# Kernel tuning notes

Measured on AMD Instinct MI355X. Metric: run time of the kernel, lower is better.

Reference implementation:

```python
import jax, jax.numpy as jnp
import numpy as np

B, C, H, W = 4, 512, 32, 32
NH = 8
HD = C // NH
PH, PW = 2, 4
NPR = PH * PW
HIDDEN = int(C * 2.0)
EPS = 1e-5

def _bn(x, p):
    g, b, m, v = p[0], p[1], p[2], p[3]
    s = g * jax.lax.rsqrt(v + EPS)
    return x * s[None, :, None, None] + (b - m * s)[None, :, None, None]

def _ln(x, p):
    mu = x.mean(-1, keepdims=True)
    var = ((x - mu) ** 2).mean(-1, keepdims=True)
    return (x - mu) * jax.lax.rsqrt(var + EPS) * p[0] + p[1]

def _dwconv(x, w):
    return jax.lax.conv_general_dilated(
        x, w, (1, 1), 'SAME',
        dimension_numbers=('NCHW', 'OIHW', 'NCHW'),
        feature_group_count=x.shape[1])

def _pw(x, w):
    # 1x1 conv, no bias: w is (O, I, 1, 1)
    return jnp.einsum('bchw,oc->bohw', x, w[:, :, 0, 0])

def _pool(x, ph, pw):
    # adaptive avg pool when output evenly divides input
    b, c, h, w = x.shape
    return x.reshape(b, c, ph, h // ph, pw, w // pw).mean(axis=(3, 5))

def _gelu(x):
    return jax.nn.gelu(x, approximate=False)

def _coords(h, w):
    y = jnp.linspace(0.0, 1.0, h)
    x = jnp.linspace(0.0, 1.0, w)
    gy, gx = jnp.meshgrid(y, x, indexing='ij')
    return jnp.stack([gy, gx], axis=-1).reshape(-1, 2)


def setup_inputs() -> dict:
    key = jax.random.key(0)
    ks = iter(jax.random.split(key, 64))
    def nrm(shape, s=0.02):
        return jax.random.normal(next(ks), shape, jnp.float32) * s
    def bnp():
        return jnp.stack([1.0 + nrm((C,), 0.1), nrm((C,), 0.1),
                          nrm((C,), 0.1), 1.0 + jnp.abs(nrm((C,), 0.2))])
    def lnp(c=C):
        return jnp.stack([jnp.ones((c,), jnp.float32), jnp.zeros((c,), jnp.float32)])
    return {
        'fused': jax.random.normal(next(ks), (B, C, H, W), jnp.float32),
        'depth': jax.random.normal(next(ks), (B, C, H, W), jnp.float32),
        'pg_dw_w': nrm((C, 1, 3, 3)), 'pg_bn1': bnp(),
        'pg_pw_w': nrm((C, C, 1, 1)), 'pg_bn2': bnp(),
        'prompt_embed': nrm((1, NPR, C)), 'pg_ln': lnp(),
        'gp_dw_w': nrm((C, 1, 3, 3)), 'gp_bn': bnp(),
        'gp_pw_w': nrm((1, C, 1, 1)), 'gp_pw_b': jnp.zeros((1,), jnp.float32),
        'gp_weight': jnp.ones((2, 1, 1, 1), jnp.float32),
        'ln1': lnp(),
        'wq': nrm((C, C)), 'wk': nrm((C, C)), 'wv': nrm((C, C)), 'wo': nrm((C, C)),
        'ln2': lnp(),
        'mlp_w1': nrm((HIDDEN, C)), 'mlp_b1': jnp.zeros((HIDDEN,), jnp.float32),
        'mlp_w2': nrm((C, HIDDEN)), 'mlp_b2': jnp.zeros((C,), jnp.float32),
        'op_dw_w': nrm((C, 1, 3, 3)), 'op_bn1': bnp(),
        'op_pw_w': nrm((C, C, 1, 1)), 'op_bn2': bnp(),
    }


def reference(fused, depth, pg_dw_w, pg_bn1, pg_pw_w, pg_bn2, prompt_embed, pg_ln,
              gp_dw_w, gp_bn, gp_pw_w, gp_pw_b, gp_weight,
              ln1, wq, wk, wv, wo, ln2, mlp_w1, mlp_b1, mlp_w2, mlp_b2,
              op_dw_w, op_bn1, op_pw_w, op_bn2):
    b = fused.shape[0]
    # --- DepthPromptGenerator ---
    pp = _gelu(_bn(_dwconv(depth, pg_dw_w), pg_bn1))
    pp = _gelu(_bn(_pw(pp, pg_pw_w), pg_bn2))
    prompt = _pool(pp, PH, PW).reshape(b, C, NPR).transpose(0, 2, 1)  # (B, P, C)
    prompt = _ln(prompt + prompt_embed, pg_ln)
    # --- GeometryPriorGenerator ---
    ds = _gelu(_bn(_dwconv(depth, gp_dw_w), gp_bn))
    ds = _pw(ds, gp_pw_w) + gp_pw_b[None, :, None, None]  # (B,1,H,W)
    img_d = ds.reshape(b, H * W)
    pr_d = _pool(ds, PH, PW).reshape(b, NPR)
    jd = jnp.concatenate([pr_d, img_d], axis=1)  # (B, N) depth scalar per token
    coords = jnp.concatenate([_coords(PH, PW), _coords(H, W)], axis=0)  # (N,2)
    pos = jnp.abs(coords[:, None, :] - coords[None, :, :]).sum(-1)  # (N,N) L1 distance
    decay = jnp.log(1.0 - 2.0 ** (-1.0 - 4.0 * jnp.arange(NH, dtype=jnp.float32) / NH))
    pos_mask = pos[None, :, :] * decay[:, None, None]  # (NH,N,N)
    depth_mask = jnp.abs(jd[:, :, None] - jd[:, None, :])[:, None, :, :] * decay[None, :, None, None]
    bias = gp_weight[0, 0, 0, 0] * pos_mask[None] + gp_weight[1, 0, 0, 0] * depth_mask  # (B,NH,N,N)
    # --- GeometryAwarePromptMixer ---
    img_tok = fused.reshape(b, C, H * W).transpose(0, 2, 1)  # (B,HW,C)
    jt = jnp.concatenate([prompt, img_tok], axis=1)  # (B,N,C)
    n = jt.shape[1]
    x = _ln(jt, ln1)
    q = jnp.einsum('bnc,dc->bnd', x, wq).reshape(b, n, NH, HD).transpose(0, 2, 1, 3)
    k = jnp.einsum('bnc,dc->bnd', x, wk).reshape(b, n, NH, HD).transpose(0, 2, 1, 3)
    v = jnp.einsum('bnc,dc->bnd', x, wv).reshape(b, n, NH, HD).transpose(0, 2, 1, 3)
    logits = jnp.einsum('bhnd,bhmd->bhnm', q, k) * (HD ** -0.5) + bias
    attn = jax.nn.softmax(logits, axis=-1)
    ao = jnp.einsum('bhnm,bhmd->bhnd', attn, v).transpose(0, 2, 1, 3).reshape(b, n, C)
    jt = jt + jnp.einsum('bnc,dc->bnd', ao, wo)
    h = _gelu(jnp.einsum('bnc,hc->bnh', _ln(jt, ln2), mlp_w1) + mlp_b1)
    jt = jt + jnp.einsum('bnh,ch->bnc', h, mlp_w2) + mlp_b2
    enh = jt[:, NPR:, :].transpose(0, 2, 1).reshape(b, C, H, W)
    # --- out_proj ---
    o = _gelu(_bn(_dwconv(enh, op_dw_w), op_bn1))
    o = _bn(_pw(o, op_pw_w), op_bn2)
    return fused + o
```

## Files before the change

kernel.cpp:

```cpp
#include <hip/hip_runtime.h>
#include <math.h>

typedef __attribute__((ext_vector_type(8))) short bf16x8;
typedef __attribute__((ext_vector_type(4))) float f32x4;

#define CH 512
#define HWP 1024
#define NTOK 1032
#define NTP 1088
#define NPRM 8
#define BB 4
#define EPSV 1e-5f
#define MTOK 4128
#define MPAD 4224
#define QSCL 0.18033688f
#define LOG2E 1.44269504f

__device__ __forceinline__ float gelu_f(float x) {
  return 0.5f * x * (1.0f + erff(x * 0.70710678118654752440f));
}

__device__ __forceinline__ ushort f2bf(float x) {
  union { float f; unsigned u; } v; v.f = x;
  unsigned r = v.u + 0x7FFF + ((v.u >> 16) & 1);
  return (ushort)(r >> 16);
}

__device__ __forceinline__ float bf2f(ushort u) {
  union { unsigned u; float f; } v; v.u = ((unsigned)u) << 16;
  return v.f;
}

__device__ __forceinline__ void gl16(const ushort* g, ushort* s) {
  __builtin_amdgcn_global_load_lds(
      (const __attribute__((address_space(1))) unsigned int*)g,
      (__attribute__((address_space(3))) unsigned int*)s,
      16, 0, 0);
}

__global__ __launch_bounds__(256) void convw(
    const float* __restrict__ wq, const float* __restrict__ wk, const float* __restrict__ wv,
    const float* __restrict__ wo, const float* __restrict__ w1, const float* __restrict__ w2,
    const float* __restrict__ pgw, const float* __restrict__ opw, const float* __restrict__ gpw,
    ushort* __restrict__ out)
{
  const int total = 2621952;
  for (int i = blockIdx.x * 256 + threadIdx.x; i < total; i += gridDim.x * 256) {
    const float* src; int off;
    if (i < 262144)       { src = wq;  off = i; }
    else if (i < 524288)  { src = wk;  off = i - 262144; }
    else if (i < 786432)  { src = wv;  off = i - 524288; }
    else if (i < 1048576) { src = wo;  off = i - 786432; }
    else if (i < 1572864) { src = w1;  off = i - 1048576; }
    else if (i < 2097152) { src = w2;  off = i - 1572864; }
    else if (i < 2359296) { src = pgw; off = i - 2097152; }
    else if (i < 2621440) { src = opw; off = i - 2359296; }
    else                  { src = gpw; off = i - 2621440; }
    out[i] = f2bf(src[off]);
  }
}

__global__ __launch_bounds__(256) void dwt_fused(
    const float* __restrict__ in, const float* __restrict__ w9p,
    const float* __restrict__ bn, ushort* __restrict__ outT)
{
  __shared__ float tile[32][33];
  const int y = blockIdx.x;
  const int c0 = blockIdx.y * 32;
  const int b = blockIdx.z;
  const int tx = threadIdx.x, ty = threadIdx.y;
  #pragma unroll
  for (int i = 0; i < 4; ++i) {
    int c = c0 + ty + i * 8;
    const float* ip = in + ((size_t)(b * CH + c)) * HWP;
    const float* wp = w9p + c * 9;
    float acc = 0.0f;
    #pragma unroll
    for (int dy = 0; dy < 3; ++dy) {
      int yy = y + dy - 1;
      if ((unsigned)yy < 32u) {
        #pragma unroll
        for (int dx = 0; dx < 3; ++dx) {
          int xx = tx + dx - 1;
          if ((unsigned)xx < 32u) acc += ip[yy * 32 + xx] * wp[dy * 3 + dx];
        }
      }
    }
    float g = bn[c], be = bn[CH + c], mm = bn[2 * CH + c], vv = bn[3 * CH + c];
    float s = g * rsqrtf(vv + EPSV);
    tile[ty + i * 8][tx] = gelu_f(acc * s + (be - mm * s));
  }
  __syncthreads();
  #pragma unroll
  for (int i = 0; i < 4; ++i)
    outT[((size_t)(b * HWP + y * 32 + ty + i * 8)) * CH + c0 + tx] = f2bf(tile[tx][ty + i * 8]);
}

__device__ __forceinline__ void stage128(const ushort* pA, const ushort* pB,
                                         ushort* lA, ushort* lB,
                                         int w, int KA, int KB)
{
  #pragma unroll
  for (int j = 0; j < 4; ++j) {
    gl16(pA + (size_t)j * 8 * KA, lA + (w * 32 + j * 8) * 64);
    gl16(pB + (size_t)j * 8 * KB, lB + (w * 32 + j * 8) * 64);
  }
}

__device__ __forceinline__ void comp128(const ushort* lA, const ushort* lB,
                                        int wm, int wn, int l, f32x4 (&acc)[4][4])
{
  #pragma unroll
  for (int ks = 0; ks < 2; ++ks) {
    int kb = ks * 4 + (l >> 4);
    int swz = ((kb ^ (l & 7)) * 8);
    bf16x8 af[4], bfv[4];
    #pragma unroll
    for (int mf = 0; mf < 4; ++mf)
      af[mf] = *(const bf16x8*)(lA + (wm + mf * 16 + (l & 15)) * 64 + swz);
    #pragma unroll
    for (int nf = 0; nf < 4; ++nf)
      bfv[nf] = *(const bf16x8*)(lB + (wn + nf * 16 + (l & 15)) * 64 + swz);
    #pragma unroll
    for (int mf = 0; mf < 4; ++mf) {
      #pragma unroll
      for (int nf = 0; nf < 4; ++nf)
        acc[mf][nf] = __builtin_amdgcn_mfma_f32_16x16x32_bf16(af[mf], bfv[nf], acc[mf][nf], 0, 0, 0);
    }
  }
}

#define G128_PRE(Abase, Bbase, KA, KB, Kdim) \
  __shared__ ushort sA[2][8192], sB[2][8192]; \
  f32x4 acc[4][4]; \
  { f32x4 z = {0.f, 0.f, 0.f, 0.f}; \
    _Pragma("unroll") for (int i = 0; i < 4; ++i) { _Pragma("unroll") for (int j = 0; j < 4; ++j) acc[i][j] = z; } } \
  const int l = threadIdx.x & 63, w = threadIdx.x >> 6; \
  const int wm = (w >> 1) * 64, wn = (w & 1) * 64; \
  const ushort* pA = (Abase) + (size_t)(w * 32 + (l >> 3)) * (KA) + ((l & 7) ^ (l >> 3)) * 8; \
  const ushort* pB = (Bbase) + (size_t)(w * 32 + (l >> 3)) * (KB) + ((l & 7) ^ (l >> 3)) * 8; \
  stage128(pA, pB, sA[0], sB[0], w, KA, KB); \
  __syncthreads(); \
  const int nk = (Kdim) / 64; \
  for (int kt = 0; kt < nk; ++kt) { \
    if (kt + 1 < nk) \
      stage128(pA + (kt + 1) * 64, pB + (kt + 1) * 64, sA[(kt + 1) & 1], sB[(kt + 1) & 1], w, KA, KB); \
    comp128(sA[kt & 1], sB[kt & 1], wm, wn, l, acc); \
    __syncthreads(); \
  }

__global__ __launch_bounds__(256) void gemm_qkv128(
    const ushort* __restrict__ A, const ushort* __restrict__ B,
    ushort* __restrict__ qh, ushort* __restrict__ kh, ushort* __restrict__ vt)
{
  const int n0 = blockIdx.x * 128, m0 = blockIdx.y * 128;
  G128_PRE(A + (size_t)m0 * 512, B + (size_t)n0 * 512, 512, 512, 512)
  #pragma unroll
  for (int nf = 0; nf < 4; ++nf) {
    int n = n0 + wn + nf * 16 + (l & 15);
    #pragma unroll
    for (int mf = 0; mf < 4; ++mf) {
      #pragma unroll
      for (int r = 0; r < 4; ++r) {
        int m = m0 + wm + mf * 16 + (l >> 4) * 4 + r;
        if (m < MTOK) {
          int b = m / NTOK;
          int tok = m - b * NTOK;
          float val = acc[mf][nf][r];
          if (n < 512) {
            qh[((size_t)((b * 8 + (n >> 6)) * NTP) + tok) * 64 + (n & 63)] = f2bf(val * QSCL);
          } else if (n < 1024) {
            int n2 = n - 512;
            kh[((size_t)((b * 8 + (n2 >> 6)) * NTP) + tok) * 64 + (n2 & 63)] = f2bf(val);
          } else {
            int n2 = n - 1024;
            vt[((size_t)((b * 8 + (n2 >> 6)) * 64) + (n2 & 63)) * NTP + tok] = f2bf(val);
          }
        }
      }
    }
  }
}

__global__ __launch_bounds__(256) void gemm_res128(
    const ushort* __restrict__ A, const ushort* __restrict__ B,
    float* __restrict__ Cf, const float* __restrict__ bias, int Kdim)
{
  const int n0 = blockIdx.x * 128, m0 = blockIdx.y * 128;
  G128_PRE(A + (size_t)m0 * Kdim, B + (size_t)n0 * Kdim, Kdim, Kdim, Kdim)
  #pragma unroll
  for (int nf = 0; nf < 4; ++nf) {
    int n = n0 + wn + nf * 16 + (l & 15);
    float bv = bias ? bias[n] : 0.0f;
    #pragma unroll
    for (int mf = 0; mf < 4; ++mf) {
      #pragma unroll
      for (int r = 0; r < 4; ++r) {
        int m = m0 + wm + mf * 16 + (l >> 4) * 4 + r;
        if (m < MTOK) Cf[(size_t)m * 512 + n] += acc[mf][nf][r] + bv;
      }
    }
  }
}

__global__ __launch_bounds__(256) void gemm_gelu128(
    const ushort* __restrict__ A, const ushort* __restrict__ B,
    const float* __restrict__ bias, ushort* __restrict__ Ob)
{
  const int n0 = blockIdx.x * 128, m0 = blockIdx.y * 128;
  G128_PRE(A + (size_t)m0 * 512, B + (size_t)n0 * 512, 512, 512, 512)
  #pragma unroll
  for (int nf = 0; nf < 4; ++nf) {
    int n = n0 + wn + nf * 16 + (l & 15);
    float bv = bias[n];
    #pragma unroll
    for (int mf = 0; mf < 4; ++mf) {
      #pragma unroll
      for (int r = 0; r < 4; ++r) {
        int m = m0 + wm + mf * 16 + (l >> 4) * 4 + r;
        if (m < MTOK) Ob[(size_t)m * 1024 + n] = f2bf(gelu_f(acc[mf][nf][r] + bv));
      }
    }
  }
}

template<int MODE>
__global__ __launch_bounds__(256) void gemm_pw128(
    const ushort* __restrict__ A, const ushort* __restrict__ B,
    const float* __restrict__ bnp, const float* __restrict__ res, float* __restrict__ Of)
{
  const int hw0 = blockIdx.x * 128, m0 = blockIdx.y * 128;
  const int b = blockIdx.z;
  G128_PRE(A + (size_t)m0 * 512, B + (size_t)(b * HWP + hw0) * 512, 512, 512, 512)
  #pragma unroll
  for (int mf = 0; mf < 4; ++mf) {
    #pragma unroll
    for (int r = 0; r < 4; ++r) {
      int o = m0 + wm + mf * 16 + (l >> 4) * 4 + r;
      float g = bnp[o], be = bnp[CH + o], mm = bnp[2 * CH + o], vv = bnp[3 * CH + o];
      float s = g * rsqrtf(vv + EPSV);
      float sh = be - mm * s;
      #pragma unroll
      for (int nf = 0; nf < 4; ++nf) {
        int hw = hw0 + wn + nf * 16 + (l & 15);
        float x = acc[mf][nf][r] * s + sh;
        size_t oi = ((size_t)(b * CH + o)) * HWP + hw;
        if (MODE == 0) Of[oi] = gelu_f(x);
        else Of[oi] = x + res[oi];
      }
    }
  }
}

__global__ __launch_bounds__(128) void pp_pool(const float* __restrict__ pp, float* __restrict__ ppool)
{
  int bc = blockIdx.x;
  int b = bc >> 9, c = bc & 511;
  __shared__ float sums[8];
  if (threadIdx.x < 8) sums[threadIdx.x] = 0.0f;
  __syncthreads();
  const float* ip = pp + (size_t)bc * HWP;
  float s0 = 0.0f, s1 = 0.0f;
  #pragma unroll
  for (int kq = 0; kq < 8; ++kq) {
    float val = ip[threadIdx.x + kq * 128];
    if (kq < 4) s0 += val; else s1 += val;
  }
  int pxr = (threadIdx.x & 31) >> 3;
  atomicAdd(&sums[pxr], s0);
  atomicAdd(&sums[4 + pxr], s1);
  __syncthreads();
  if (threadIdx.x < 8)
    ppool[((size_t)b * 8 + threadIdx.x) * CH + c] = sums[threadIdx.x] * (1.0f / 128.0f);
}

__global__ __launch_bounds__(128) void prompt_ln(
    const float* __restrict__ ppool, const float* __restrict__ embed,
    const float* __restrict__ lnp, float* __restrict__ jt)
{
  int rB = blockIdx.x;
  int b = rB >> 3, pI = rB & 7;
  float4 val = ((const float4*)(ppool + (size_t)rB * CH))[threadIdx.x];
  float4 e = ((const float4*)(embed + (size_t)pI * CH))[threadIdx.x];
  val.x += e.x; val.y += e.y; val.z += e.z; val.w += e.w;
  float sum = val.x + val.y + val.z + val.w;
  float sq = val.x * val.x + val.y * val.y + val.z * val.z + val.w * val.w;
  #pragma unroll
  for (int off = 1; off < 64; off <<= 1) { sum += __shfl_xor(sum, off); sq += __shfl_xor(sq, off); }
  __shared__ float s2[4];
  if ((threadIdx.x & 63) == 0) { s2[(threadIdx.x >> 6) * 2] = sum; s2[(threadIdx.x >> 6) * 2 + 1] = sq; }
  __syncthreads();
  sum = s2[0] + s2[2]; sq = s2[1] + s2[3];
  float mu = sum * (1.0f / 512.0f);
  float var = sq * (1.0f / 512.0f) - mu * mu;
  float rstd = rsqrtf(var + EPSV);
  int c = threadIdx.x * 4;
  float4 o;
  o.x = (val.x - mu) * rstd * lnp[c] + lnp[CH + c];
  o.y = (val.y - mu) * rstd * lnp[c + 1] + lnp[CH + c + 1];
  o.z = (val.z - mu) * rstd * lnp[c + 2] + lnp[CH + c + 2];
  o.w = (val.w - mu) * rstd * lnp[c + 3] + lnp[CH + c + 3];
  ((float4*)(jt + ((size_t)(b * NTOK + pI)) * CH))[threadIdx.x] = o;
}

__global__ __launch_bounds__(256) void gp_dot(
    const ushort* __restrict__ xT, const ushort* __restrict__ wbf,
    const float* __restrict__ b0, float* __restrict__ jdv)
{
  const int b = blockIdx.y;
  const int row0 = blockIdx.x * 16;
  const int l = threadIdx.x & 63, w = threadIdx.x >> 6;
  bf16x8 wv = *(const bf16x8*)(wbf + l * 8);
  float wf[8];
  #pragma unroll
  for (int j = 0; j < 8; ++j) wf[j] = bf2f((ushort)wv[j]);
  #pragma unroll
  for (int rr = 0; rr < 4; ++rr) {
    int hw = row0 + w * 4 + rr;
    bf16x8 xv = *(const bf16x8*)(xT + ((size_t)(b * HWP + hw)) * CH + l * 8);
    float s = 0.0f;
    #pragma unroll
    for (int j = 0; j < 8; ++j) s += wf[j] * bf2f((ushort)xv[j]);
    #pragma unroll
    for (int off = 1; off < 64; off <<= 1) s += __shfl_xor(s, off);
    if (l == 0) jdv[b * NTP + NPRM + hw] = s + b0[0];
  }
}

__global__ __launch_bounds__(256) void jd_pool(float* jd)
{
  int b = blockIdx.x;
  __shared__ float sums[8];
  if (threadIdx.x < 8) sums[threadIdx.x] = 0.0f;
  __syncthreads();
  #pragma unroll
  for (int kq = 0; kq < 4; ++kq) {
    int px = threadIdx.x + kq * 256;
    int y = px >> 5, x = px & 31;
    int r = (y >> 4) * 4 + (x >> 3);
    atomicAdd(&sums[r], jd[b * NTP + NPRM + px]);
  }
  __syncthreads();
  if (threadIdx.x < 8) jd[b * NTP + threadIdx.x] = sums[threadIdx.x] * (1.0f / 128.0f);
}

__global__ __launch_bounds__(256) void img_to_tokens(const float* __restrict__ fused, float* __restrict__ jt)
{
  __shared__ float tile[32][33];
  int hw0 = blockIdx.x * 32, c0 = blockIdx.y * 32, b = blockIdx.z;
  int tx = threadIdx.x, ty = threadIdx.y;
  #pragma unroll
  for (int i = 0; i < 4; ++i)
    tile[ty + i * 8][tx] = fused[((size_t)(b * CH + c0 + ty + i * 8)) * HWP + hw0 + tx];
  __syncthreads();
  #pragma unroll
  for (int i = 0; i < 4; ++i)
    jt[((size_t)(b * NTOK + NPRM + hw0 + ty + i * 8)) * CH + c0 + tx] = tile[tx][ty + i * 8];
}

__global__ __launch_bounds__(256) void tokens_to_img(const float* __restrict__ jt, float* __restrict__ out)
{
  __shared__ float tile[32][33];
  int hw0 = blockIdx.x * 32, c0 = blockIdx.y * 32, b = blockIdx.z;
  int tx = threadIdx.x, ty = threadIdx.y;
  #pragma unroll
  for (int i = 0; i < 4; ++i)
    tile[ty + i * 8][tx] = jt[((size_t)(b * NTOK + NPRM + hw0 + ty + i * 8)) * CH + c0 + tx];
  __syncthreads();
  #pragma unroll
  for (int i = 0; i < 4; ++i)
    out[((size_t)(b * CH + c0 + ty + i * 8)) * HWP + hw0 + tx] = tile[tx][ty + i * 8];
}

__global__ __launch_bounds__(128) void ln_rows_bf(
    const float* __restrict__ in, const float* __restrict__ lnp, ushort* __restrict__ out)
{
  int row = blockIdx.x;
  float4 val = ((const float4*)(in + (size_t)row * CH))[threadIdx.x];
  float sum = val.x + val.y + val.z + val.w;
  float sq = val.x * val.x + val.y * val.y + val.z * val.z + val.w * val.w;
  #pragma unroll
  for (int off = 1; off < 64; off <<= 1) { sum += __shfl_xor(sum, off); sq += __shfl_xor(sq, off); }
  __shared__ float s2[4];
  if ((threadIdx.x & 63) == 0) { s2[(threadIdx.x >> 6) * 2] = sum; s2[(threadIdx.x >> 6) * 2 + 1] = sq; }
  __syncthreads();
  sum = s2[0] + s2[2]; sq = s2[1] + s2[3];
  float mu = sum * (1.0f / 512.0f);
  float var = sq * (1.0f / 512.0f) - mu * mu;
  float rstd = rsqrtf(var + EPSV);
  int c = threadIdx.x * 4;
  ushort4 o;
  o.x = f2bf((val.x - mu) * rstd * lnp[c] + lnp[CH + c]);
  o.y = f2bf((val.y - mu) * rstd * lnp[c + 1] + lnp[CH + c + 1]);
  o.z = f2bf((val.z - mu) * rstd * lnp[c + 2] + lnp[CH + c + 2]);
  o.w = f2bf((val.w - mu) * rstd * lnp[c + 3] + lnp[CH + c + 3]);
  *(ushort4*)(out + (size_t)row * CH + c) = o;
}

__device__ __forceinline__ void tok_coord(int idx, float& y, float& x)
{
  if (idx < NPRM) { y = (float)(idx >> 2); x = (float)(idx & 3) * (1.0f / 3.0f); }
  else { int t = idx - NPRM; y = (float)(t >> 5) * (1.0f / 31.0f); x = (float)(t & 31) * (1.0f / 31.0f); }
}

__global__ __launch_bounds__(256) void attn_mfma2(
    const ushort* __restrict__ qh, const ushort* __restrict__ kh,
    const ushort* __restrict__ vT, const float* __restrict__ jd,
    const float* __restrict__ gw, ushort* __restrict__ ao)
{
  __shared__ ushort sK[8192], sV[8192];
  __shared__ ushort Pl[4][16][72];
  const int t = threadIdx.x, l = t & 63, w = t >> 6;
  const int h = blockIdx.y, b = blockIdx.z;
  const int i0 = blockIdx.x * 64 + w * 16;
  const ushort* Q = qh + (size_t)(b * 8 + h) * NTP * 64;
  const ushort* K = kh + (size_t)(b * 8 + h) * NTP * 64;
  const ushort* V = vT + (size_t)(b * 8 + h) * 64 * NTP;
  const float decay = logf(1.0f - exp2f(-1.0f - 0.5f * (float)h)) * LOG2E;
  const float g0 = gw[0] * decay, g1 = gw[1] * decay;

  bf16x8 qf0 = *(const bf16x8*)(Q + (size_t)(i0 + (l & 15)) * 64 + (l >> 4) * 8);
  bf16x8 qf1 = *(const bf16x8*)(Q + (size_t)(i0 + (l & 15)) * 64 + 32 + (l >> 4) * 8);

  float yi[4], xi[4], jdi[4];
  #pragma unroll
  for (int r = 0; r < 4; ++r) {
    int i = i0 + (l >> 4) * 4 + r;
    tok_coord(i, yi[r], xi[r]);
    jdi[r] = jd[b * NTP + i];
  }

  float m_r[4] = { -1e30f, -1e30f, -1e30f, -1e30f };
  float l_r[4] = { 0.f, 0.f, 0.f, 0.f };
  f32x4 of[4];
  { f32x4 z = {0.f, 0.f, 0.f, 0.f};
    #pragma unroll
    for (int d = 0; d < 4; ++d) of[d] = z; }

#define ASTAGE(buf, j0s) { \
    const ushort* gk = K + (size_t)((j0s) + l) * 64; \
    const ushort* gv = V + (size_t)l * NTP + (j0s); \
    gl16(gk + w * 8,       sK + (buf) * 4096 + w * 512); \
    gl16(gk + (w + 4) * 8, sK + (buf) * 4096 + (w + 4) * 512); \
    gl16(gv + w * 8,       sV + (buf) * 4096 + w * 512); \
    gl16(gv + (w + 4) * 8, sV + (buf) * 4096 + (w + 4) * 512); }

  ASTAGE(0, 0)
  __syncthreads();
  const int NJT = 17;
  for (int jti = 0; jti < NJT; ++jti) {
    const int j0 = jti * 64;
    if (jti + 1 < NJT) ASTAGE((jti + 1) & 1, j0 + 64)
    const ushort* bK = sK + (jti & 1) * 4096;
    const ushort* bV = sV + (jti & 1) * 4096;

    f32x4 sfr[4];
    #pragma unroll
    for (int jf = 0; jf < 4; ++jf) {
      bf16x8 k0 = *(const bf16x8*)(bK + (((l >> 4)) * 64 + jf * 16 + (l & 15)) * 8);
      bf16x8 k1 = *(const bf16x8*)(bK + ((4 + (l >> 4)) * 64 + jf * 16 + (l & 15)) * 8);
      f32x4 z = {0.f, 0.f, 0.f, 0.f};
      z = __builtin_amdgcn_mfma_f32_16x16x32_bf16(qf0, k0, z, 0, 0, 0);
      z = __builtin_amdgcn_mfma_f32_16x16x32_bf16(qf1, k1, z, 0, 0, 0);
      sfr[jf] = z;
    }
    float pvv[4][4];
    float mt[4] = { -1e30f, -1e30f, -1e30f, -1e30f };
    #pragma unroll
    for (int jf = 0; jf < 4; ++jf) {
      int jj = j0 + jf * 16 + (l & 15);
      float yj, xj;
      tok_coord(jj, yj, xj);
      float jdj = jd[b * NTP + jj];
      bool valid = jj < NTOK;
      #pragma unroll
      for (int r = 0; r < 4; ++r) {
        float bias = g0 * (fabsf(yi[r] - yj) + fabsf(xi[r] - xj)) + g1 * fabsf(jdi[r] - jdj);
        float sv = valid ? (sfr[jf][r] + bias) : -1e30f;
        pvv[jf][r] = sv;
        mt[r] = fmaxf(mt[r], sv);
      }
    }
    #pragma unroll
    for (int r = 0; r < 4; ++r) {
      #pragma unroll
      for (int off = 1; off < 16; off <<= 1) mt[r] = fmaxf(mt[r], __shfl_xor(mt[r], off));
    }
    float alpha[4], ls[4];
    #pragma unroll
    for (int r = 0; r < 4; ++r) {
      float mn = fmaxf(m_r[r], mt[r]);
      alpha[r] = exp2f(m_r[r] - mn);
      m_r[r] = mn;
      ls[r] = 0.f;
    }
    #pragma unroll
    for (int jf = 0; jf < 4; ++jf) {
      #pragma unroll
      for (int r = 0; r < 4; ++r) {
        float pp = exp2f(pvv[jf][r] - m_r[r]);
        pvv[jf][r] = pp;
        ls[r] += pp;
      }
    }
    #pragma unroll
    for (int r = 0; r < 4; ++r) {
      #pragma unroll
      for (int off = 1; off < 16; off <<= 1) ls[r] += __shfl_xor(ls[r], off);
      l_r[r] = l_r[r] * alpha[r] + ls[r];
    }
    #pragma unroll
    for (int d = 0; d < 4; ++d) {
      #pragma unroll
      for (int r = 0; r < 4; ++r) of[d][r] *= alpha[r];
    }
    #pragma unroll
    for (int jf = 0; jf < 4; ++jf) {
      #pragma unroll
      for (int r = 0; r < 4; ++r)
        Pl[w][(l >> 4) * 4 + r][jf * 16 + (l & 15)] = f2bf(pvv[jf][r]);
    }
    asm volatile("s_waitcnt lgkmcnt(0)" ::: "memory");
    bf16x8 pa0 = *(const bf16x8*)&Pl[w][l & 15][(l >> 4) * 8];
    bf16x8 pa1 = *(const bf16x8*)&Pl[w][l & 15][32 + (l >> 4) * 8];
    #pragma unroll
    for (int df = 0; df < 4; ++df) {
      bf16x8 v0 = *(const bf16x8*)(bV + (((l >> 4)) * 64 + df * 16 + (l & 15)) * 8);
      bf16x8 v1 = *(const bf16x8*)(bV + ((4 + (l >> 4)) * 64 + df * 16 + (l & 15)) * 8);
      of[df] = __builtin_amdgcn_mfma_f32_16x16x32_bf16(pa0, v0, of[df], 0, 0, 0);
      of[df] = __builtin_amdgcn_mfma_f32_16x16x32_bf16(pa1, v1, of[df], 0, 0, 0);
    }
    __syncthreads();
  }
  #pragma unroll
  for (int r = 0; r < 4; ++r) {
    int i = i0 + (l >> 4) * 4 + r;
    if (i < NTOK) {
      float inv = 1.0f / l_r[r];
      #pragma unroll
      for (int df = 0; df < 4; ++df)
        ao[((size_t)(b * NTOK + i)) * 512 + h * 64 + df * 16 + (l & 15)] = f2bf(of[df][r] * inv);
    }
  }
}

extern "C" void kernel_launch(void* const* d_in, const int* in_sizes, int n_in,
                              void* d_out, int out_size, void* d_ws, size_t ws_size,
                              hipStream_t stream)
{
  const float* fused = (const float*)d_in[0];
  const float* depth = (const float*)d_in[1];
  const float* pg_dw_w = (const float*)d_in[2];
  const float* pg_bn1 = (const float*)d_in[3];
  const float* pg_pw_w = (const float*)d_in[4];
  const float* pg_bn2 = (const float*)d_in[5];
  const float* prompt_embed = (const float*)d_in[6];
  const float* pg_ln = (const float*)d_in[7];
  const float* gp_dw_w = (const float*)d_in[8];
  const float* gp_bn = (const float*)d_in[9];
  const float* gp_pw_w = (const float*)d_in[10];
  const float* gp_pw_b = (const float*)d_in[11];
  const float* gp_weight = (const float*)d_in[12];
  const float* ln1 = (const float*)d_in[13];
  const float* wq = (const float*)d_in[14];
  const float* wk = (const float*)d_in[15];
  const float* wv = (const float*)d_in[16];
  const float* wo = (const float*)d_in[17];
  const float* ln2 = (const float*)d_in[18];
  const float* mlp_w1 = (const float*)d_in[19];
  const float* mlp_b1 = (const float*)d_in[20];
  const float* mlp_w2 = (const float*)d_in[21];
  const float* mlp_b2 = (const float*)d_in[22];
  const float* op_dw_w = (const float*)d_in[23];
  const float* op_bn1 = (const float*)d_in[24];
  const float* op_pw_w = (const float*)d_in[25];
  const float* op_bn2 = (const float*)d_in[26];
  float* out = (float*)d_out;

  char* p = (char*)d_ws;
  auto alloc = [&](size_t bytes) { char* r = p; p += (bytes + 1023) & ~(size_t)1023; return r; };
  float*  jt    = (float*) alloc((size_t)MTOK * 512 * 4);
  ushort* xb    = (ushort*)alloc((size_t)MPAD * 512 * 2);
  ushort* hb    = (ushort*)alloc((size_t)MPAD * 1024 * 2);
  ushort* ao    = (ushort*)alloc((size_t)MPAD * 512 * 2);
  ushort* qhB   = (ushort*)alloc((size_t)32 * NTP * 64 * 2);
  ushort* khB   = (ushort*)alloc((size_t)32 * NTP * 64 * 2);
  ushort* vTB   = (ushort*)alloc((size_t)32 * NTP * 64 * 2);
  ushort* dwT1  = (ushort*)alloc((size_t)BB * HWP * CH * 2);
  ushort* dwT2  = (ushort*)alloc((size_t)BB * HWP * CH * 2);
  float*  ppf   = (float*) alloc((size_t)BB * CH * HWP * 4);
  float*  Bf    = (float*) alloc((size_t)BB * CH * HWP * 4);
  float*  jdv   = (float*) alloc((size_t)BB * NTP * 4);
  float*  ppool = (float*) alloc((size_t)BB * 8 * CH * 4);
  ushort* wbf   = (ushort*)alloc((size_t)2621952 * 2);

  ushort* wqkv_bf = wbf;
  ushort* wo_bf   = wbf + 786432;
  ushort* w1_bf   = wbf + 1048576;
  ushort* w2_bf   = wbf + 1572864;
  ushort* pgw_bf  = wbf + 2097152;
  ushort* opw_bf  = wbf + 2359296;
  ushort* gpw_bf  = wbf + 2621440;

  hipLaunchKernelGGL(convw, dim3(4096), dim3(256), 0, stream,
                     wq, wk, wv, wo, mlp_w1, mlp_w2, pg_pw_w, op_pw_w, gp_pw_w, wbf);

  hipLaunchKernelGGL(dwt_fused, dim3(32, 16, BB), dim3(32, 8), 0, stream, depth, pg_dw_w, pg_bn1, dwT1);
  hipLaunchKernelGGL(gemm_pw128<0>, dim3(8, 4, BB), dim3(256), 0, stream, pgw_bf, dwT1, pg_bn2, (const float*)nullptr, ppf);
  hipLaunchKernelGGL(pp_pool, dim3(BB * CH), dim3(128), 0, stream, ppf, ppool);
  hipLaunchKernelGGL(prompt_ln, dim3(BB * NPRM), dim3(128), 0, stream, ppool, prompt_embed, pg_ln, jt);

  hipLaunchKernelGGL(dwt_fused, dim3(32, 16, BB), dim3(32, 8), 0, stream, depth, gp_dw_w, gp_bn, dwT2);
  hipLaunchKernelGGL(gp_dot, dim3(64, BB), dim3(256), 0, stream, dwT2, gpw_bf, gp_pw_b, jdv);
  hipLaunchKernelGGL(jd_pool, dim3(BB), dim3(256), 0, stream, jdv);

  hipLaunchKernelGGL(img_to_tokens, dim3(32, 16, BB), dim3(32, 8), 0, stream, fused, jt);
  hipLaunchKernelGGL(ln_rows_bf, dim3(MTOK), dim3(128), 0, stream, jt, ln1, xb);
  hipLaunchKernelGGL(gemm_qkv128, dim3(12, 33), dim3(256), 0, stream, xb, wqkv_bf, qhB, khB, vTB);
  hipLaunchKernelGGL(attn_mfma2, dim3(17, 8, BB), dim3(256), 0, stream, qhB, khB, vTB, jdv, gp_weight, ao);
  hipLaunchKernelGGL(gemm_res128, dim3(4, 33), dim3(256), 0, stream, ao, wo_bf, jt, (const float*)nullptr, 512);
  hipLaunchKernelGGL(ln_rows_bf, dim3(MTOK), dim3(128), 0, stream, jt, ln2, xb);
  hipLaunchKernelGGL(gemm_gelu128, dim3(8, 33), dim3(256), 0, stream, xb, w1_bf, mlp_b1, hb);
  hipLaunchKernelGGL(gemm_res128, dim3(4, 33), dim3(256), 0, stream, hb, w2_bf, jt, mlp_b2, 1024);

  hipLaunchKernelGGL(tokens_to_img, dim3(32, 16, BB), dim3(32, 8), 0, stream, jt, Bf);
  hipLaunchKernelGGL(dwt_fused, dim3(32, 16, BB), dim3(32, 8), 0, stream, Bf, op_dw_w, op_bn1, dwT1);
  hipLaunchKernelGGL(gemm_pw128<1>, dim3(8, 4, BB), dim3(256), 0, stream, opw_bf, dwT1, op_bn2, fused, out);
}
```

Baseline: 390.3 us.

## Fuse preprocessing stages: dual depthwise conv, pooled pointwise GEMM, combined token/LN kernel

Computes both depthwise convolutions on the depth input in one pass and fuses the prompt pointwise GEMM with GELU and region pooling through shared-memory and global atomics, so the full-resolution fp32 intermediate is never written. It also merges image-to-token transpose, LN1, prompt LN, the geometry dot product and its pooling into one multi-role kernel. The output depthwise conv now reads the token layout directly, dropping the tokens-to-image transpose. The convw grid is halved and zeroing memsets are added. These changes cut kernel launches and large fp32 round trips, at the cost of atomic contention, float-atomic ordering nondeterminism, and a combined kernel whose roles are unevenly loaded.

```diff
diff --git a/kernel.cpp b/kernel.cpp
--- a/kernel.cpp
+++ b/kernel.cpp
@@ -60,11 +60,14 @@
   }
 }
 
-__global__ __launch_bounds__(256) void dwt_fused(
-    const float* __restrict__ in, const float* __restrict__ w9p,
-    const float* __restrict__ bn, ushort* __restrict__ outT)
-{
-  __shared__ float tile[32][33];
+__global__ __launch_bounds__(256) void dwt_dual(
+    const float* __restrict__ in,
+    const float* __restrict__ w1p, const float* __restrict__ bn1,
+    const float* __restrict__ w2p, const float* __restrict__ bn2,
+    ushort* __restrict__ o1, ushort* __restrict__ o2)
+{
+  __shared__ float t1[32][33];
+  __shared__ float t2[32][33];
   const int y = blockIdx.x;
   const int c0 = blockIdx.y * 32;
   const int b = blockIdx.z;
@@ -73,8 +76,9 @@
   for (int i = 0; i < 4; ++i) {
     int c = c0 + ty + i * 8;
     const float* ip = in + ((size_t)(b * CH + c)) * HWP;
-    const float* wp = w9p + c * 9;
-    float acc = 0.0f;
+    const float* wa = w1p + c * 9;
+    const float* wb = w2p + c * 9;
+    float a1 = 0.0f, a2 = 0.0f;
     #pragma unroll
     for (int dy = 0; dy < 3; ++dy) {
       int yy = y + dy - 1;
@@ -82,18 +86,28 @@
         #pragma unroll
         for (int dx = 0; dx < 3; ++dx) {
           int xx = tx + dx - 1;
-          if ((unsigned)xx < 32u) acc += ip[yy * 32 + xx] * wp[dy * 3 + dx];
+          if ((unsigned)xx < 32u) {
+            float v = ip[yy * 32 + xx];
+            a1 += v * wa[dy * 3 + dx];
+            a2 += v * wb[dy * 3 + dx];
+          }
         }
       }
     }
-    float g = bn[c], be = bn[CH + c], mm = bn[2 * CH + c], vv = bn[3 * CH + c];
-    float s = g * rsqrtf(vv + EPSV);
-    tile[ty + i * 8][tx] = gelu_f(acc * s + (be - mm * s));
+    float g1 = bn1[c], be1 = bn1[CH + c], m1 = bn1[2 * CH + c], v1 = bn1[3 * CH + c];
+    float s1 = g1 * rsqrtf(v1 + EPSV);
+    t1[ty + i * 8][tx] = gelu_f(a1 * s1 + (be1 - m1 * s1));
+    float g2 = bn2[c], be2 = bn2[CH + c], m2 = bn2[2 * CH + c], v2 = bn2[3 * CH + c];
+    float s2 = g2 * rsqrtf(v2 + EPSV);
+    t2[ty + i * 8][tx] = gelu_f(a2 * s2 + (be2 - m2 * s2));
   }
   __syncthreads();
   #pragma unroll
-  for (int i = 0; i < 4; ++i)
-    outT[((size_t)(b * HWP + y * 32 + ty + i * 8)) * CH + c0 + tx] = f2bf(tile[tx][ty + i * 8]);
+  for (int i = 0; i < 4; ++i) {
+    size_t row = (size_t)(b * HWP + y * 32 + ty + i * 8) * CH + c0 + tx;
+    o1[row] = f2bf(t1[tx][ty + i * 8]);
+    o2[row] = f2bf(t2[tx][ty + i * 8]);
+  }
 }
 
 __device__ __forceinline__ void stage128(const ushort* pA, const ushort* pB,
@@ -224,8 +238,53 @@
   }
 }
 
-template<int MODE>
-__global__ __launch_bounds__(256) void gemm_pw128(
+__global__ __launch_bounds__(256) void gemm_pw_pool(
+    const ushort* __restrict__ A, const ushort* __restrict__ B,
+    const float* __restrict__ bnp, float* __restrict__ ppool)
+{
+  __shared__ float poolL[8][128];
+  const int hw0 = blockIdx.x * 128, m0 = blockIdx.y * 128;
+  const int b = blockIdx.z;
+  {
+    int t = threadIdx.x;
+    #pragma unroll
+    for (int k = 0; k < 4; ++k) { int idx = t + k * 256; poolL[idx >> 7][idx & 127] = 0.0f; }
+  }
+  G128_PRE(A + (size_t)m0 * 512, B + (size_t)(b * HWP + hw0) * 512, 512, 512, 512)
+  #pragma unroll
+  for (int mf = 0; mf < 4; ++mf) {
+    #pragma unroll
+    for (int r = 0; r < 4; ++r) {
+      int ol = wm + mf * 16 + (l >> 4) * 4 + r;
+      int o = m0 + ol;
+      float g = bnp[o], be = bnp[CH + o], mm = bnp[2 * CH + o], vv = bnp[3 * CH + o];
+      float s = g * rsqrtf(vv + EPSV);
+      float sh = be - mm * s;
+      #pragma unroll
+      for (int nf = 0; nf < 4; ++nf) {
+        int hw = hw0 + wn + nf * 16 + (l & 15);
+        float x = gelu_f(acc[mf][nf][r] * s + sh);
+        int y = hw >> 5, xx = hw & 31;
+        int rg = (y >> 4) * 4 + (xx >> 3);
+        atomicAdd(&poolL[rg][ol], x);
+      }
+    }
+  }
+  __syncthreads();
+  {
+    int t = threadIdx.x;
+    #pragma unroll
+    for (int k = 0; k < 4; ++k) {
+      int idx = t + k * 256;
+      int rg = idx >> 7, oo = idx & 127;
+      float v = poolL[rg][oo];
+      if (v != 0.0f)
+        atomicAdd(&ppool[((size_t)(b * 8 + rg)) * 512 + m0 + oo], v * (1.0f / 128.0f));
+    }
+  }
+}
+
+__global__ __launch_bounds__(256) void gemm_pw_res(
     const ushort* __restrict__ A, const ushort* __restrict__ B,
     const float* __restrict__ bnp, const float* __restrict__ res, float* __restrict__ Of)
 {
@@ -243,133 +302,116 @@
       #pragma unroll
       for (int nf = 0; nf < 4; ++nf) {
         int hw = hw0 + wn + nf * 16 + (l & 15);
-        float x = acc[mf][nf][r] * s + sh;
         size_t oi = ((size_t)(b * CH + o)) * HWP + hw;
-        if (MODE == 0) Of[oi] = gelu_f(x);
-        else Of[oi] = x + res[oi];
-      }
-    }
-  }
-}
-
-__global__ __launch_bounds__(128) void pp_pool(const float* __restrict__ pp, float* __restrict__ ppool)
-{
-  int bc = blockIdx.x;
-  int b = bc >> 9, c = bc & 511;
-  __shared__ float sums[8];
-  if (threadIdx.x < 8) sums[threadIdx.x] = 0.0f;
-  __syncthreads();
-  const float* ip = pp + (size_t)bc * HWP;
-  float s0 = 0.0f, s1 = 0.0f;
-  #pragma unroll
-  for (int kq = 0; kq < 8; ++kq) {
-    float val = ip[threadIdx.x + kq * 128];
-    if (kq < 4) s0 += val; else s1 += val;
-  }
-  int pxr = (threadIdx.x & 31) >> 3;
-  atomicAdd(&sums[pxr], s0);
-  atomicAdd(&sums[4 + pxr], s1);
-  __syncthreads();
-  if (threadIdx.x < 8)
-    ppool[((size_t)b * 8 + threadIdx.x) * CH + c] = sums[threadIdx.x] * (1.0f / 128.0f);
-}
-
-__global__ __launch_bounds__(128) void prompt_ln(
-    const float* __restrict__ ppool, const float* __restrict__ embed,
-    const float* __restrict__ lnp, float* __restrict__ jt)
-{
-  int rB = blockIdx.x;
-  int b = rB >> 3, pI = rB & 7;
-  float4 val = ((const float4*)(ppool + (size_t)rB * CH))[threadIdx.x];
-  float4 e = ((const float4*)(embed + (size_t)pI * CH))[threadIdx.x];
-  val.x += e.x; val.y += e.y; val.z += e.z; val.w += e.w;
-  float sum = val.x + val.y + val.z + val.w;
-  float sq = val.x * val.x + val.y * val.y + val.z * val.z + val.w * val.w;
-  #pragma unroll
-  for (int off = 1; off < 64; off <<= 1) { sum += __shfl_xor(sum, off); sq += __shfl_xor(sq, off); }
-  __shared__ float s2[4];
-  if ((threadIdx.x & 63) == 0) { s2[(threadIdx.x >> 6) * 2] = sum; s2[(threadIdx.x >> 6) * 2 + 1] = sq; }
-  __syncthreads();
-  sum = s2[0] + s2[2]; sq = s2[1] + s2[3];
-  float mu = sum * (1.0f / 512.0f);
-  float var = sq * (1.0f / 512.0f) - mu * mu;
-  float rstd = rsqrtf(var + EPSV);
-  int c = threadIdx.x * 4;
-  float4 o;
-  o.x = (val.x - mu) * rstd * lnp[c] + lnp[CH + c];
-  o.y = (val.y - mu) * rstd * lnp[c + 1] + lnp[CH + c + 1];
-  o.z = (val.z - mu) * rstd * lnp[c + 2] + lnp[CH + c + 2];
-  o.w = (val.w - mu) * rstd * lnp[c + 3] + lnp[CH + c + 3];
-  ((float4*)(jt + ((size_t)(b * NTOK + pI)) * CH))[threadIdx.x] = o;
-}
-
-__global__ __launch_bounds__(256) void gp_dot(
-    const ushort* __restrict__ xT, const ushort* __restrict__ wbf,
+        Of[oi] = acc[mf][nf][r] * s + sh + res[oi];
+      }
+    }
+  }
+}
+
+__global__ __launch_bounds__(256) void combo_mid(
+    const float* __restrict__ fused, const float* __restrict__ ppool,
+    const float* __restrict__ embed, const float* __restrict__ pgln,
+    const float* __restrict__ ln1, float* __restrict__ jt, ushort* __restrict__ xb,
+    const ushort* __restrict__ dwT2, const ushort* __restrict__ gpw,
     const float* __restrict__ b0, float* __restrict__ jdv)
 {
-  const int b = blockIdx.y;
-  const int row0 = blockIdx.x * 16;
-  const int l = threadIdx.x & 63, w = threadIdx.x >> 6;
-  bf16x8 wv = *(const bf16x8*)(wbf + l * 8);
-  float wf[8];
-  #pragma unroll
-  for (int j = 0; j < 8; ++j) wf[j] = bf2f((ushort)wv[j]);
-  #pragma unroll
-  for (int rr = 0; rr < 4; ++rr) {
-    int hw = row0 + w * 4 + rr;
-    bf16x8 xv = *(const bf16x8*)(xT + ((size_t)(b * HWP + hw)) * CH + l * 8);
-    float s = 0.0f;
-    #pragma unroll
-    for (int j = 0; j < 8; ++j) s += wf[j] * bf2f((ushort)xv[j]);
-    #pragma unroll
-    for (int off = 1; off < 64; off <<= 1) s += __shfl_xor(s, off);
-    if (l == 0) jdv[b * NTP + NPRM + hw] = s + b0[0];
-  }
-}
-
-__global__ __launch_bounds__(256) void jd_pool(float* jd)
-{
-  int b = blockIdx.x;
-  __shared__ float sums[8];
-  if (threadIdx.x < 8) sums[threadIdx.x] = 0.0f;
-  __syncthreads();
-  #pragma unroll
-  for (int kq = 0; kq < 4; ++kq) {
-    int px = threadIdx.x + kq * 256;
-    int y = px >> 5, x = px & 31;
-    int r = (y >> 4) * 4 + (x >> 3);
-    atomicAdd(&sums[r], jd[b * NTP + NPRM + px]);
-  }
-  __syncthreads();
-  if (threadIdx.x < 8) jd[b * NTP + threadIdx.x] = sums[threadIdx.x] * (1.0f / 128.0f);
-}
-
-__global__ __launch_bounds__(256) void img_to_tokens(const float* __restrict__ fused, float* __restrict__ jt)
-{
-  __shared__ float tile[32][33];
-  int hw0 = blockIdx.x * 32, c0 = blockIdx.y * 32, b = blockIdx.z;
-  int tx = threadIdx.x, ty = threadIdx.y;
-  #pragma unroll
-  for (int i = 0; i < 4; ++i)
-    tile[ty + i * 8][tx] = fused[((size_t)(b * CH + c0 + ty + i * 8)) * HWP + hw0 + tx];
-  __syncthreads();
-  #pragma unroll
-  for (int i = 0; i < 4; ++i)
-    jt[((size_t)(b * NTOK + NPRM + hw0 + ty + i * 8)) * CH + c0 + tx] = tile[tx][ty + i * 8];
-}
-
-__global__ __launch_bounds__(256) void tokens_to_img(const float* __restrict__ jt, float* __restrict__ out)
-{
-  __shared__ float tile[32][33];
-  int hw0 = blockIdx.x * 32, c0 = blockIdx.y * 32, b = blockIdx.z;
-  int tx = threadIdx.x, ty = threadIdx.y;
-  #pragma unroll
-  for (int i = 0; i < 4; ++i)
-    tile[ty + i * 8][tx] = jt[((size_t)(b * NTOK + NPRM + hw0 + ty + i * 8)) * CH + c0 + tx];
-  __syncthreads();
-  #pragma unroll
-  for (int i = 0; i < 4; ++i)
-    out[((size_t)(b * CH + c0 + ty + i * 8)) * HWP + hw0 + tx] = tile[tx][ty + i * 8];
+  __shared__ float T[32][513];
+  __shared__ float red[16];
+  const int t = threadIdx.x;
+  const int bx = blockIdx.x;
+  if (bx < 128) {
+    int b = bx >> 5, hw0 = (bx & 31) * 32;
+    int tx = t & 31, ty = t >> 5;
+    #pragma unroll
+    for (int cc = 0; cc < 512; cc += 8)
+      T[tx][cc + ty] = fused[((size_t)(b * 512 + cc + ty)) * 1024 + hw0 + tx];
+    __syncthreads();
+    int tok = t >> 3, j = t & 7;
+    float s = 0.f, sq = 0.f;
+    #pragma unroll
+    for (int i = 0; i < 64; ++i) {
+      float v = T[tok][j * 64 + i];
+      s += v; sq += v * v;
+    }
+    s += __shfl_xor(s, 1); sq += __shfl_xor(sq, 1);
+    s += __shfl_xor(s, 2); sq += __shfl_xor(sq, 2);
+    s += __shfl_xor(s, 4); sq += __shfl_xor(sq, 4);
+    float mu = s * (1.f / 512.f);
+    float var = sq * (1.f / 512.f) - mu * mu;
+    float rstd = rsqrtf(var + EPSV);
+    size_t row = (size_t)(b * NTOK + NPRM + hw0 + tok);
+    #pragma unroll
+    for (int i = 0; i < 64; i += 4) {
+      int c = j * 64 + i;
+      float4 v4;
+      v4.x = T[tok][c]; v4.y = T[tok][c + 1]; v4.z = T[tok][c + 2]; v4.w = T[tok][c + 3];
+      *(float4*)(jt + row * 512 + c) = v4;
+      ushort4 u;
+      u.x = f2bf((v4.x - mu) * rstd * ln1[c] + ln1[512 + c]);
+      u.y = f2bf((v4.y - mu) * rstd * ln1[c + 1] + ln1[512 + c + 1]);
+      u.z = f2bf((v4.z - mu) * rstd * ln1[c + 2] + ln1[512 + c + 2]);
+      u.w = f2bf((v4.w - mu) * rstd * ln1[c + 3] + ln1[512 + c + 3]);
+      *(ushort4*)(xb + row * 512 + c) = u;
+    }
+  } else if (bx < 160) {
+    int idx = bx - 128, b = idx >> 3, pI = idx & 7;
+    int c = t * 2;
+    float2 v = *(const float2*)(ppool + ((size_t)(b * 8 + pI)) * 512 + c);
+    float2 e = *(const float2*)(embed + pI * 512 + c);
+    v.x += e.x; v.y += e.y;
+    float s = v.x + v.y, sq = v.x * v.x + v.y * v.y;
+    #pragma unroll
+    for (int off = 1; off < 64; off <<= 1) { s += __shfl_xor(s, off); sq += __shfl_xor(sq, off); }
+    if ((t & 63) == 0) { red[(t >> 6) * 2] = s; red[(t >> 6) * 2 + 1] = sq; }
+    __syncthreads();
+    s = red[0] + red[2] + red[4] + red[6];
+    sq = red[1] + red[3] + red[5] + red[7];
+    float mu = s * (1.f / 512.f);
+    float rstd = rsqrtf(sq * (1.f / 512.f) - mu * mu + EPSV);
+    float o0 = (v.x - mu) * rstd * pgln[c] + pgln[512 + c];
+    float o1 = (v.y - mu) * rstd * pgln[c + 1] + pgln[512 + c + 1];
+    size_t row = (size_t)(b * NTOK + pI);
+    jt[row * 512 + c] = o0;
+    jt[row * 512 + c + 1] = o1;
+    float s2 = o0 + o1, sq2 = o0 * o0 + o1 * o1;
+    #pragma unroll
+    for (int off = 1; off < 64; off <<= 1) { s2 += __shfl_xor(s2, off); sq2 += __shfl_xor(sq2, off); }
+    if ((t & 63) == 0) { red[8 + (t >> 6) * 2] = s2; red[9 + (t >> 6) * 2] = sq2; }
+    __syncthreads();
+    s2 = red[8] + red[10] + red[12] + red[14];
+    sq2 = red[9] + red[11] + red[13] + red[15];
+    float mu2 = s2 * (1.f / 512.f);
+    float rstd2 = rsqrtf(sq2 * (1.f / 512.f) - mu2 * mu2 + EPSV);
+    xb[row * 512 + c]     = f2bf((o0 - mu2) * rstd2 * ln1[c] + ln1[512 + c]);
+    xb[row * 512 + c + 1] = f2bf((o1 - mu2) * rstd2 * ln1[c + 1] + ln1[512 + c + 1]);
+  } else {
+    int idx = bx - 160;
+    int b = idx >> 6, row0 = (idx & 63) * 16;
+    int l = t & 63, w = t >> 6;
+    bf16x8 wv = *(const bf16x8*)(gpw + l * 8);
+    float wf[8];
+    #pragma unroll
+    for (int j = 0; j < 8; ++j) wf[j] = bf2f((ushort)wv[j]);
+    float bias0 = b0[0];
+    #pragma unroll
+    for (int rr = 0; rr < 4; ++rr) {
+      int hw = row0 + w * 4 + rr;
+      bf16x8 xv = *(const bf16x8*)(dwT2 + ((size_t)(b * HWP + hw)) * CH + l * 8);
+      float s = 0.0f;
+      #pragma unroll
+      for (int j = 0; j < 8; ++j) s += wf[j] * bf2f((ushort)xv[j]);
+      #pragma unroll
+      for (int off = 1; off < 64; off <<= 1) s += __shfl_xor(s, off);
+      if (l == 0) {
+        float sf = s + bias0;
+        jdv[b * NTP + NPRM + hw] = sf;
+        int y = hw >> 5, xx = hw & 31;
+        int rg = (y >> 4) * 4 + (xx >> 3);
+        atomicAdd(&jdv[b * NTP + rg], sf * (1.0f / 128.0f));
+      }
+    }
+  }
 }
 
 __global__ __launch_bounds__(128) void ln_rows_bf(
@@ -395,6 +437,50 @@
   o.z = f2bf((val.z - mu) * rstd * lnp[c + 2] + lnp[CH + c + 2]);
   o.w = f2bf((val.w - mu) * rstd * lnp[c + 3] + lnp[CH + c + 3]);
   *(ushort4*)(out + (size_t)row * CH + c) = o;
+}
+
+__global__ __launch_bounds__(256) void dwt_op(
+    const float* __restrict__ jt, const float* __restrict__ w9p,
+    const float* __restrict__ bn, ushort* __restrict__ outT)
+{
+  __shared__ float Tt[3][32][33];
+  const int y = blockIdx.x;
+  const int c0 = blockIdx.y * 32;
+  const int b = blockIdx.z;
+  const int tx = threadIdx.x, ty = threadIdx.y;
+  #pragma unroll
+  for (int ry = 0; ry < 3; ++ry) {
+    int yy = y - 1 + ry;
+    bool ok = (unsigned)yy < 32u;
+    #pragma unroll
+    for (int it = 0; it < 4; ++it) {
+      int px = ty + it * 8;
+      float v = ok ? jt[((size_t)(b * NTOK + NPRM + yy * 32 + px)) * 512 + c0 + tx] : 0.0f;
+      Tt[ry][px][tx] = v;
+    }
+  }
+  __syncthreads();
+  int c = c0 + tx;
+  float w9[9];
+  #pragma unroll
+  for (int k = 0; k < 9; ++k) w9[k] = w9p[c * 9 + k];
+  float g = bn[c], be = bn[CH + c], mm = bn[2 * CH + c], vv = bn[3 * CH + c];
+  float s = g * rsqrtf(vv + EPSV);
+  float sh = be - mm * s;
+  #pragma unroll
+  for (int it = 0; it < 4; ++it) {
+    int px = ty + it * 8;
+    float acc = 0.0f;
+    #pragma unroll
+    for (int dy = 0; dy < 3; ++dy) {
+      #pragma unroll
+      for (int dx = 0; dx < 3; ++dx) {
+        int xx = px + dx - 1;
+        if ((unsigned)xx < 32u) acc += Tt[dy][xx][tx] * w9[dy * 3 + dx];
+      }
+    }
+    outT[((size_t)(b * HWP + y * 32 + px)) * CH + c] = f2bf(gelu_f(acc * s + sh));
+  }
 }
 
 __device__ __forceinline__ void tok_coord(int idx, float& y, float& x)
@@ -579,6 +665,8 @@
 
   char* p = (char*)d_ws;
   auto alloc = [&](size_t bytes) { char* r = p; p += (bytes + 1023) & ~(size_t)1023; return r; };
+  float*  jdv   = (float*) alloc((size_t)BB * NTP * 4);
+  float*  ppool = (float*) alloc((size_t)BB * 8 * CH * 4);
   float*  jt    = (float*) alloc((size_t)MTOK * 512 * 4);
   ushort* xb    = (ushort*)alloc((size_t)MPAD * 512 * 2);
   ushort* hb    = (ushort*)alloc((size_t)MPAD * 1024 * 2);
@@ -588,10 +676,6 @@
   ushort* vTB   = (ushort*)alloc((size_t)32 * NTP * 64 * 2);
   ushort* dwT1  = (ushort*)alloc((size_t)BB * HWP * CH * 2);
   ushort* dwT2  = (ushort*)alloc((size_t)BB * HWP * CH * 2);
-  float*  ppf   = (float*) alloc((size_t)BB * CH * HWP * 4);
-  float*  Bf    = (float*) alloc((size_t)BB * CH * HWP * 4);
-  float*  jdv   = (float*) alloc((size_t)BB * NTP * 4);
-  float*  ppool = (float*) alloc((size_t)BB * 8 * CH * 4);
   ushort* wbf   = (ushort*)alloc((size_t)2621952 * 2);
 
   ushort* wqkv_bf = wbf;
@@ -602,28 +686,23 @@
   ushort* opw_bf  = wbf + 2359296;
   ushort* gpw_bf  = wbf + 2621440;
 
-  hipLaunchKernelGGL(convw, dim3(4096), dim3(256), 0, stream,
+  hipMemsetAsync(jdv, 0, (size_t)BB * NTP * 4 + 1024  + (size_t)BB * 8 * CH * 4 - 1024, stream);
+  hipMemsetAsync(ppool, 0, (size_t)BB * 8 * CH * 4, stream);
+
+  hipLaunchKernelGGL(convw, dim3(2048), dim3(256), 0, stream,
                      wq, wk, wv, wo, mlp_w1, mlp_w2, pg_pw_w, op_pw_w, gp_pw_w, wbf);
 
-  hipLaunchKernelGGL(dwt_fused, dim3(32, 16, BB), dim3(32, 8), 0, stream, depth, pg_dw_w, pg_bn1, dwT1);
-  hipLaunchKernelGGL(gemm_pw128<0>, dim3(8, 4, BB), dim3(256), 0, stream, pgw_bf, dwT1, pg_bn2, (const float*)nullptr, ppf);
-  hipLaunchKernelGGL(pp_pool, dim3(BB * CH), dim3(128), 0, stream, ppf, ppool);
-  hipLaunchKernelGGL(prompt_ln, dim3(BB * NPRM), dim3(128), 0, stream, ppool, prompt_embed, pg_ln, jt);
-
-  hipLaunchKernelGGL(dwt_fused, dim3(32, 16, BB), dim3(32, 8), 0, stream, depth, gp_dw_w, gp_bn, dwT2);
-  hipLaunchKernelGGL(gp_dot, dim3(64, BB), dim3(256), 0, stream, dwT2, gpw_bf, gp_pw_b, jdv);
-  hipLaunchKernelGGL(jd_pool, dim3(BB), dim3(256), 0, stream, jdv);
-
-  hipLaunchKernelGGL(img_to_tokens, dim3(32, 16, BB), dim3(32, 8), 0, stream, fused, jt);
-  hipLaunchKernelGGL(ln_rows_bf, dim3(MTOK), dim3(128), 0, stream, jt, ln1, xb);
+  hipLaunchKernelGGL(dwt_dual, dim3(32, 16, BB), dim3(32, 8), 0, stream,
+                     depth, pg_dw_w, pg_bn1, gp_dw_w, gp_bn, dwT1, dwT2);
+  hipLaunchKernelGGL(gemm_pw_pool, dim3(8, 4, BB), dim3(256), 0, stream, pgw_bf, dwT1, pg_bn2, ppool);
+  hipLaunchKernelGGL(combo_mid, dim3(416), dim3(256), 0, stream,
+                     fused, ppool, prompt_embed, pg_ln, ln1, jt, xb, dwT2, gpw_bf, gp_pw_b, jdv);
   hipLaunchKernelGGL(gemm_qkv128, dim3(12, 33), dim3(256), 0, stream, xb, wqkv_bf, qhB, khB, vTB);
   hipLaunchKernelGGL(attn_mfma2, dim3(17, 8, BB), dim3(256), 0, stream, qhB, khB, vTB, jdv, gp_weight, ao);
   hipLaunchKernelGGL(gemm_res128, dim3(4, 33), dim3(256), 0, stream, ao, wo_bf, jt, (const float*)nullptr, 512);
   hipLaunchKernelGGL(ln_rows_bf, dim3(MTOK), dim3(128), 0, stream, jt, ln2, xb);
   hipLaunchKernelGGL(gemm_gelu128, dim3(8, 33), dim3(256), 0, stream, xb, w1_bf, mlp_b1, hb);
   hipLaunchKernelGGL(gemm_res128, dim3(4, 33), dim3(256), 0, stream, hb, w2_bf, jt, mlp_b2, 1024);
-
-  hipLaunchKernelGGL(tokens_to_img, dim3(32, 16, BB), dim3(32, 8), 0, stream, jt, Bf);
-  hipLaunchKernelGGL(dwt_fused, dim3(32, 16, BB), dim3(32, 8), 0, stream, Bf, op_dw_w, op_bn1, dwT1);
-  hipLaunchKernelGGL(gemm_pw128<1>, dim3(8, 4, BB), dim3(256), 0, stream, opw_bf, dwT1, op_bn2, fused, out);
-}
+  hipLaunchKernelGGL(dwt_op, dim3(32, 16, BB), dim3(32, 8), 0, stream, jt, op_dw_w, op_bn1, dwT1);
+  hipLaunchKernelGGL(gemm_pw_res, dim3(8, 4, BB), dim3(256), 0, stream, opw_bf, dwT1, op_bn2, fused, out);
+}
```

After: 388.3 us. No clear change (-0.5%).
